# Kernel optimization log

Measured on AMD Instinct MI355X. Metric: run time of the kernel, lower is better.

Reference implementation:

```python
import jax, jax.numpy as jnp
import numpy as np

N = 1048576   # total nodes
E = 8388608   # total edges
IN = 5        # in_channels
H = 32        # hid_channels
G = 16384     # num graphs
C = 10        # num_classes
L = 2         # conv_unit
EPS = 1e-5


def setup_inputs() -> dict:
    key = jax.random.key(0)
    ks = jax.random.split(key, 16)
    x = jax.random.normal(ks[0], (N, IN), dtype=jnp.float32)
    edge_index = jax.random.randint(ks[1], (2, E), 0, N, dtype=jnp.int64)
    edge_attr = jax.random.uniform(ks[2], (E, 1), dtype=jnp.float32)
    batch = jnp.sort(jax.random.randint(ks[3], (N,), 0, G, dtype=jnp.int64))
    s_in = 1.0 / np.sqrt(IN)
    s_h = 1.0 / np.sqrt(H)
    s_2h = 1.0 / np.sqrt(2 * H)
    W_emb = jax.random.normal(ks[4], (H, IN), dtype=jnp.float32) * s_in
    b_emb = jnp.zeros((H,), dtype=jnp.float32)
    W_rel = jax.random.normal(ks[5], (L, H, H), dtype=jnp.float32) * s_h
    b_rel = jnp.zeros((L, H), dtype=jnp.float32)
    W_root = jax.random.normal(ks[6], (L, H, H), dtype=jnp.float32) * s_h
    bn_gamma = jnp.ones((L, H), dtype=jnp.float32)
    bn_beta = jnp.zeros((L, H), dtype=jnp.float32)
    W1 = jax.random.normal(ks[7], (2 * H, H), dtype=jnp.float32) * s_h
    b1 = jnp.zeros((2 * H,), dtype=jnp.float32)
    W2 = jax.random.normal(ks[8], (C, 2 * H), dtype=jnp.float32) * s_2h
    b2 = jnp.zeros((C,), dtype=jnp.float32)
    return {
        "x": x, "edge_index": edge_index, "edge_attr": edge_attr, "batch": batch,
        "W_emb": W_emb, "b_emb": b_emb, "W_rel": W_rel, "b_rel": b_rel,
        "W_root": W_root, "bn_gamma": bn_gamma, "bn_beta": bn_beta,
        "W1": W1, "b1": b1, "W2": W2, "b2": b2,
    }


def _graph_conv(x, src, dst, ew, Wrel, brel, Wroot):
    # PyG GraphConv: lin_rel(scatter_add(ew * x[src] -> dst)) + lin_root(x)
    msg = x[src] * ew[:, None]                              # [E, H]
    agg = jax.ops.segment_sum(msg, dst, num_segments=N)     # [N, H]
    return agg @ Wrel.T + brel + x @ Wroot.T


def _batch_norm(x, gamma, beta):
    mean = jnp.mean(x, axis=0)
    var = jnp.mean(jnp.square(x - mean), axis=0)  # biased, as torch training BN
    return (x - mean) * jax.lax.rsqrt(var + EPS) * gamma + beta


def reference(x, edge_index, edge_attr, batch, W_emb, b_emb, W_rel, b_rel,
              W_root, bn_gamma, bn_beta, W1, b1, W2, b2):
    src, dst = edge_index[0], edge_index[1]
    ew = edge_attr.reshape(-1)
    h = x @ W_emb.T + b_emb                                  # node_emb
    for i in range(L):
        h = _graph_conv(h, src, dst, ew, W_rel[i], b_rel[i], W_root[i])
        h = jax.nn.relu(_batch_norm(h, bn_gamma[i], bn_beta[i]))
    graph_x = jax.ops.segment_max(h, batch, num_segments=G)  # global_max_pool
    hidden = jax.nn.relu(graph_x @ W1.T + b1)
    return hidden @ W2.T + b2                                # [G, C]
```

## Files before the change

kernel.cpp:

```cpp
#include <hip/hip_runtime.h>
#include <hip/hip_fp16.h>

#define NN 1048576
#define NE 8388608
#define NG 16384
#define NBUCK 256
#define BSH 12
#define EPB (NE / 256)

typedef _Float16 half8 __attribute__((ext_vector_type(8)));
typedef float f32x16 __attribute__((ext_vector_type(16)));

__global__ __launch_bounds__(256) void k_embed(const float* __restrict__ x,
    const float* __restrict__ W, const float* __restrict__ b, __half* __restrict__ h) {
  __shared__ float sW[160];
  __shared__ float sb[32];
  int t = threadIdx.x;
  if (t < 160) sW[t] = W[t];
  if (t < 32) sb[t] = b[t];
  __syncthreads();
  int idx = blockIdx.x * 256 + t;
  int c = idx & 31, n = idx >> 5;
  const float* xr = x + n * 5;
  float acc = sb[c];
#pragma unroll
  for (int k = 0; k < 5; ++k) acc = fmaf(xr[k], sW[c * 5 + k], acc);
  h[idx] = __float2half(acc);
}

__global__ __launch_bounds__(256) void k_pcnt(const int* __restrict__ dst, int* __restrict__ hist) {
  __shared__ int lh[NBUCK];
  int t = threadIdx.x;
  lh[t] = 0;
  __syncthreads();
  int base = blockIdx.x * EPB;
  for (int e = base + t; e < base + EPB; e += 256)
    atomicAdd(&lh[dst[e] >> BSH], 1);
  __syncthreads();
  hist[t * 256 + blockIdx.x] = lh[t];
}

__global__ __launch_bounds__(256) void k_scanA(int* __restrict__ hist, int* __restrict__ tot) {
  __shared__ int s2[256];
  int b = blockIdx.x, t = threadIdx.x;
  int v = hist[b * 256 + t];
  s2[t] = v; __syncthreads();
  for (int st = 1; st < 256; st <<= 1) {
    int a = (t >= st) ? s2[t - st] : 0; __syncthreads(); s2[t] += a; __syncthreads();
  }
  hist[b * 256 + t] = s2[t] - v;
  if (t == 255) tot[b] = s2[255];
}

__global__ __launch_bounds__(256) void k_scanB(const int* __restrict__ tot, int* __restrict__ gbase) {
  __shared__ int s2[256];
  int t = threadIdx.x;
  int c = tot[t];
  s2[t] = c; __syncthreads();
  for (int st = 1; st < 256; st <<= 1) {
    int a = (t >= st) ? s2[t - st] : 0; __syncthreads(); s2[t] += a; __syncthreads();
  }
  gbase[t] = s2[t] - c;
  if (t == 255) gbase[256] = s2[255];
}

__global__ __launch_bounds__(256) void k_part(const int* __restrict__ ei, const float* __restrict__ ew,
                                              const int* __restrict__ hist, const int* __restrict__ gbase,
                                              uint2* __restrict__ bsw) {
  __shared__ int cur[NBUCK];
  int t = threadIdx.x, blk = blockIdx.x;
  cur[t] = gbase[t] + hist[t * 256 + blk];
  __syncthreads();
  int base = blk * EPB;
  for (int e = base + t; e < base + EPB; e += 256) {
    int src = ei[e];
    int d   = ei[NE + e];
    unsigned wb = __float_as_uint(ew[e]);
    int b = d >> BSH;
    int pos = atomicAdd(&cur[b], 1);
    bsw[pos] = make_uint2(((unsigned)src << 12) | (unsigned)(d & 4095), wb);
  }
}

__global__ __launch_bounds__(256) void k_fillD(const int* __restrict__ gbase, const uint2* __restrict__ bsw,
                                               int* __restrict__ rowptr, uint2* __restrict__ colw) {
  __shared__ int loc[4096];
  __shared__ int s2[256];
  int t = threadIdx.x, b = blockIdx.x;
  int beg = gbase[b], end = gbase[b + 1], gb = beg;
  int node_base = b << BSH;
#pragma unroll
  for (int j = 0; j < 16; ++j) loc[t * 16 + j] = 0;
  __syncthreads();
  for (int i = beg + t; i < end; i += 256) atomicAdd(&loc[bsw[i].x & 4095], 1);
  __syncthreads();
  int v[16]; int tsum = 0;
#pragma unroll
  for (int j = 0; j < 16; ++j) { v[j] = loc[t * 16 + j]; tsum += v[j]; }
  s2[t] = tsum; __syncthreads();
  for (int st = 1; st < 256; st <<= 1) {
    int a = (t >= st) ? s2[t - st] : 0; __syncthreads(); s2[t] += a; __syncthreads();
  }
  int run = s2[t] - tsum;
#pragma unroll
  for (int j = 0; j < 16; ++j) {
    loc[t * 16 + j] = run;
    rowptr[node_base + t * 16 + j] = gb + run;
    run += v[j];
  }
  if (b == NBUCK - 1 && t == 255) rowptr[NN] = NE;
  __syncthreads();
  for (int i = beg + t; i < end; i += 256) {
    uint2 r = bsw[i];
    int p = atomicAdd(&loc[r.x & 4095], 1);
    colw[gb + p] = make_uint2(r.x >> 12, r.y);
  }
}

__global__ __launch_bounds__(256) void k_gbound(const int* __restrict__ batch, int* __restrict__ gptr) {
  int n = blockIdx.x * 256 + threadIdx.x;
  int b = batch[n];
  int prev = (n == 0) ? -1 : batch[n - 1];
  for (int g = prev + 1; g <= b; ++g) gptr[g] = n;
  if (n == NN - 1) {
    for (int g = b + 1; g <= NG; ++g) gptr[g] = NN;
  }
}

template <int FUSE_BN>
__global__ __launch_bounds__(256) void k_agglin(
    const int* __restrict__ rowptr, const uint2* __restrict__ colw,
    const __half* __restrict__ hIn, const float* __restrict__ bnss,
    const float* __restrict__ Wrel, const float* __restrict__ brel,
    const float* __restrict__ Wroot, __half* __restrict__ hPre,
    double* __restrict__ stats) {
  __shared__ __half sA[4][1024];
  __shared__ uint2 sE[256];
  __shared__ float sBn[64];
  __shared__ double rS[256], rQ[256];
  int t = threadIdx.x;
  int wv = t >> 6, lane = t & 63;
  int c = lane & 31, hi = lane >> 5, grp = t >> 5;
  char* myA = (char*)sA[wv];

  if (FUSE_BN && t < 64) sBn[t] = bnss[t];
  __syncthreads();

  float bs0 = 0.f, bs1 = 0.f;
  if constexpr (FUSE_BN) { bs0 = bnss[c]; bs1 = bnss[32 + c]; }

  half8 bfr[4];
#pragma unroll
  for (int m = 0; m < 4; ++m)
#pragma unroll
    for (int j = 0; j < 8; ++j) {
      int k = 16 * m + hi * 8 + j;
      float w = (k < 32) ? Wrel[c * 32 + k] : Wroot[c * 32 + (k - 32)];
      bfr[m][j] = (_Float16)w;
    }
  float bias = brel[c];
  double aS = 0.0, aQ = 0.0;

  for (int tile = blockIdx.x * 4 + wv; tile < NN / 32; tile += gridDim.x * 4) {
    int nbase = tile * 32;
    for (int r = 0; r < 16; ++r) {
      int node = 2 * r + hi;
      int n = nbase + node;
      int r0 = rowptr[n], r1 = rowptr[n + 1];
      float acc = 0.f;
      for (int j = r0; j < r1; j += 32) {
        int m_ = r1 - j; if (m_ > 32) m_ = 32;
        uint2 cw = make_uint2(0u, 0u);
        if (c < m_) cw = colw[j + c];
        sE[t] = cw;
        int mm = (m_ + 7) & ~7;
        for (int i = 0; i < mm; i += 8) {
          const uint4* eb4 = (const uint4*)&sE[grp * 32 + i];
          uint4 q0 = eb4[0], q1 = eb4[1], q2 = eb4[2], q3 = eb4[3];
          float h0 = __half2float(hIn[(size_t)q0.x * 32 + c]);
          float h1 = __half2float(hIn[(size_t)q0.z * 32 + c]);
          float h2 = __half2float(hIn[(size_t)q1.x * 32 + c]);
          float h3 = __half2float(hIn[(size_t)q1.z * 32 + c]);
          float h4 = __half2float(hIn[(size_t)q2.x * 32 + c]);
          float h5 = __half2float(hIn[(size_t)q2.z * 32 + c]);
          float h6 = __half2float(hIn[(size_t)q3.x * 32 + c]);
          float h7 = __half2float(hIn[(size_t)q3.z * 32 + c]);
          if constexpr (FUSE_BN) {
            h0 = fmaxf(fmaf(h0, bs0, bs1), 0.f);
            h1 = fmaxf(fmaf(h1, bs0, bs1), 0.f);
            h2 = fmaxf(fmaf(h2, bs0, bs1), 0.f);
            h3 = fmaxf(fmaf(h3, bs0, bs1), 0.f);
            h4 = fmaxf(fmaf(h4, bs0, bs1), 0.f);
            h5 = fmaxf(fmaf(h5, bs0, bs1), 0.f);
            h6 = fmaxf(fmaf(h6, bs0, bs1), 0.f);
            h7 = fmaxf(fmaf(h7, bs0, bs1), 0.f);
          }
          acc = fmaf(__uint_as_float(q0.y), h0, acc);
          acc = fmaf(__uint_as_float(q0.w), h1, acc);
          acc = fmaf(__uint_as_float(q1.y), h2, acc);
          acc = fmaf(__uint_as_float(q1.w), h3, acc);
          acc = fmaf(__uint_as_float(q2.y), h4, acc);
          acc = fmaf(__uint_as_float(q2.w), h5, acc);
          acc = fmaf(__uint_as_float(q3.y), h6, acc);
          acc = fmaf(__uint_as_float(q3.w), h7, acc);
        }
      }
      int bw = (node * 64 + c * 2) ^ ((node & 7) << 4);
      *(__half*)(myA + bw) = __float2half(acc);
    }
    f32x16 d;
#pragma unroll
    for (int r = 0; r < 16; ++r) d[r] = bias;
#pragma unroll
    for (int m = 0; m < 4; ++m) {
      half8 a;
      if (m < 2) {
        int node = c;
        int br = (node * 64 + (16 * m + hi * 8) * 2) ^ ((node & 7) << 4);
        a = *(const half8*)(myA + br);
      } else {
        int chb = 16 * (m - 2) + hi * 8;
        a = *(const half8*)(hIn + (size_t)(nbase + c) * 32 + chb);
        if constexpr (FUSE_BN) {
#pragma unroll
          for (int j = 0; j < 8; ++j) {
            float v = (float)a[j];
            v = fmaxf(fmaf(v, sBn[chb + j], sBn[32 + chb + j]), 0.f);
            a[j] = (_Float16)v;
          }
        }
      }
      d = __builtin_amdgcn_mfma_f32_32x32x16_f16(a, bfr[m], d, 0, 0, 0);
    }
#pragma unroll
    for (int r = 0; r < 16; ++r) {
      int node = (r & 3) + 8 * (r >> 2) + 4 * hi;
      float v = d[r];
      hPre[(size_t)(nbase + node) * 32 + c] = __float2half(v);
      aS += v; aQ += (double)v * v;
    }
  }
  rS[t] = aS; rQ[t] = aQ;
  __syncthreads();
  for (int s = 128; s >= 32; s >>= 1) {
    if (t < s) { rS[t] += rS[t + s]; rQ[t] += rQ[t + s]; }
    __syncthreads();
  }
  if (t < 32) {
    atomicAdd(&stats[t], rS[t]);
    atomicAdd(&stats[32 + t], rQ[t]);
  }
}

__global__ void k_bnfin(const double* __restrict__ stats, const float* __restrict__ gamma,
                        const float* __restrict__ beta, float* __restrict__ ss) {
  int c = threadIdx.x;
  double mean = stats[c] * (1.0 / NN);
  double var = stats[32 + c] * (1.0 / NN) - mean * mean;
  float scale = gamma[c] * (float)(1.0 / sqrt(var + 1e-5));
  ss[c] = scale;
  ss[32 + c] = beta[c] - (float)mean * scale;
}

__global__ __launch_bounds__(256) void k_pool(const __half* __restrict__ hB,
    const float* __restrict__ ss, const int* __restrict__ gptr, float* __restrict__ pooled) {
  int t = threadIdx.x;
  int wv = t >> 6, lane = t & 63;
  int p = lane >> 4, cl = lane & 15;
  float s0x = ss[2 * cl], s0y = ss[2 * cl + 1];
  float s1x = ss[32 + 2 * cl], s1y = ss[32 + 2 * cl + 1];
  int g = blockIdx.x * 4 + wv;
  int a = gptr[g], b = gptr[g + 1];
  float mx = 0.f, my = 0.f;
  for (int n = a + p; n < b; n += 4) {
    float2 hv = __half22float2(*(const __half2*)(hB + (size_t)n * 32 + 2 * cl));
    mx = fmaxf(mx, fmaf(hv.x, s0x, s1x));
    my = fmaxf(my, fmaf(hv.y, s0y, s1y));
  }
  mx = fmaxf(mx, __shfl_xor(mx, 16, 64)); my = fmaxf(my, __shfl_xor(my, 16, 64));
  mx = fmaxf(mx, __shfl_xor(mx, 32, 64)); my = fmaxf(my, __shfl_xor(my, 32, 64));
  if (p == 0) *(float2*)&pooled[g * 32 + 2 * cl] = make_float2(mx, my);
}

__global__ __launch_bounds__(256) void k_head(const float* __restrict__ pooled,
    const float* __restrict__ W1, const float* __restrict__ b1,
    const float* __restrict__ W2, const float* __restrict__ b2, float* __restrict__ out) {
  __shared__ float sW1[64 * 33], sW2[10 * 65], sb1[64], sb2[10];
  __shared__ float sHid[4][64];
  int t = threadIdx.x;
  for (int i = t; i < 2048; i += 256) sW1[(i >> 5) * 33 + (i & 31)] = W1[i];
  for (int i = t; i < 640; i += 256) sW2[(i >> 6) * 65 + (i & 63)] = W2[i];
  if (t < 64) sb1[t] = b1[t];
  if (t < 10) sb2[t] = b2[t];
  __syncthreads();
  int w = t >> 6, lane = t & 63;
  for (int g = blockIdx.x * 4 + w; g < NG; g += gridDim.x * 4) {
    float pv = (lane < 32) ? pooled[g * 32 + lane] : 0.f;
    float acc = sb1[lane];
#pragma unroll
    for (int k = 0; k < 32; ++k)
      acc = fmaf(__shfl(pv, k, 64), sW1[lane * 33 + k], acc);
    acc = fmaxf(acc, 0.f);
    sHid[w][lane] = acc;
    __syncthreads();
    if (lane < 10) {
      float o = sb2[lane];
#pragma unroll
      for (int j = 0; j < 64; ++j) o = fmaf(sHid[w][j], sW2[lane * 65 + j], o);
      out[g * 10 + lane] = o;
    }
    __syncthreads();
  }
}

extern "C" void kernel_launch(void* const* d_in, const int* in_sizes, int n_in,
                              void* d_out, int out_size, void* d_ws, size_t ws_size,
                              hipStream_t stream) {
  const float* x      = (const float*)d_in[0];
  const int*   ei     = (const int*)d_in[1];
  const float* ea     = (const float*)d_in[2];
  const int*   batch  = (const int*)d_in[3];
  const float* W_emb  = (const float*)d_in[4];
  const float* b_emb  = (const float*)d_in[5];
  const float* W_rel  = (const float*)d_in[6];
  const float* b_rel  = (const float*)d_in[7];
  const float* W_root = (const float*)d_in[8];
  const float* gamma  = (const float*)d_in[9];
  const float* beta   = (const float*)d_in[10];
  const float* W1     = (const float*)d_in[11];
  const float* b1     = (const float*)d_in[12];
  const float* W2     = (const float*)d_in[13];
  const float* b2     = (const float*)d_in[14];
  float* out = (float*)d_out;

  char* ws = (char*)d_ws;
  size_t off = 0;
  __half* hA    = (__half*)(ws + off); off += (size_t)NN * 32 * 2;
  uint2*  colw  = (uint2*)(ws + off);  off += (size_t)NE * 8;
  uint2*  bsw   = (uint2*)(ws + off);
  __half* hB    = (__half*)(ws + off);
  off += (size_t)NE * 8;
  int*    rowptr= (int*)(ws + off);    off += ((size_t)NN + 64) * 4;
  int*    hist  = (int*)(ws + off);    off += (size_t)NBUCK * 256 * 4;
  int*    tot   = (int*)(ws + off);    off += 1024;
  int*    gbase = (int*)(ws + off);    off += 2048;
  int*    gptr  = (int*)(ws + off);    off += ((size_t)NG + 64) * 4;
  float*  pooled= (float*)(ws + off);
  double* stats = (double*)d_out;
  float*  ss0   = (float*)((char*)d_out + 512);
  float*  ss1   = (float*)((char*)d_out + 768);

  k_embed<<<NN * 32 / 256, 256, 0, stream>>>(x, W_emb, b_emb, hA);

  k_pcnt <<<256, 256, 0, stream>>>(ei + NE, hist);
  k_scanA<<<NBUCK, 256, 0, stream>>>(hist, tot);
  k_scanB<<<1, 256, 0, stream>>>(tot, gbase);
  k_part <<<256, 256, 0, stream>>>(ei, ea, hist, gbase, bsw);
  k_fillD<<<NBUCK, 256, 0, stream>>>(gbase, bsw, rowptr, colw);
  k_gbound<<<NN / 256, 256, 0, stream>>>(batch, gptr);

  (void)hipMemsetAsync(stats, 0, 64 * 8, stream);
  k_agglin<0><<<2048, 256, 0, stream>>>(rowptr, colw, hA, nullptr,
                                        W_rel, b_rel, W_root, hB, stats);
  k_bnfin<<<1, 32, 0, stream>>>(stats, gamma, beta, ss0);

  (void)hipMemsetAsync(stats, 0, 64 * 8, stream);
  k_agglin<1><<<2048, 256, 0, stream>>>(rowptr, colw, hB, ss0,
                                        W_rel + 1024, b_rel + 32, W_root + 1024, hA, stats);
  k_bnfin<<<1, 32, 0, stream>>>(stats, gamma + 32, beta + 32, ss1);

  k_pool<<<NG / 4, 256, 0, stream>>>(hA, ss1, gptr, pooled);
  k_head<<<1024, 256, 0, stream>>>(pooled, W1, b1, W2, b2, out);
}
```

Before: 1.007 ms.

## Prefetch rowptr and next node's edge chunk; use float per-thread BN stats

```diff
diff --git a/kernel.cpp b/kernel.cpp
--- a/kernel.cpp
+++ b/kernel.cpp
@@ -128,7 +128,7 @@
 }
 
 template <int FUSE_BN>
-__global__ __launch_bounds__(256) void k_agglin(
+__global__ __launch_bounds__(256, 8) void k_agglin(
     const int* __restrict__ rowptr, const uint2* __restrict__ colw,
     const __half* __restrict__ hIn, const float* __restrict__ bnss,
     const float* __restrict__ Wrel, const float* __restrict__ brel,
@@ -159,20 +159,30 @@
       bfr[m][j] = (_Float16)w;
     }
   float bias = brel[c];
-  double aS = 0.0, aQ = 0.0;
+  float aS = 0.f, aQ = 0.f;
 
   for (int tile = blockIdx.x * 4 + wv; tile < NN / 32; tile += gridDim.x * 4) {
     int nbase = tile * 32;
+    int rp = 0;
+    if (lane < 33) rp = rowptr[nbase + lane];
+    int r0 = __shfl(rp, hi, 64);
+    int r1 = __shfl(rp, hi + 1, 64);
+    uint2 cw = make_uint2(0u, 0u);
+    { int m_ = r1 - r0; if (m_ > 32) m_ = 32; if (c < m_) cw = colw[r0 + c]; }
+
     for (int r = 0; r < 16; ++r) {
-      int node = 2 * r + hi;
-      int n = nbase + node;
-      int r0 = rowptr[n], r1 = rowptr[n + 1];
+      sE[t] = cw;
+      int sr0 = r0, sr1 = r1;
+      if (r < 15) {
+        r0 = __shfl(rp, 2 * (r + 1) + hi, 64);
+        r1 = __shfl(rp, 2 * (r + 1) + hi + 1, 64);
+        cw = make_uint2(0u, 0u);
+        int m_ = r1 - r0; if (m_ > 32) m_ = 32;
+        if (c < m_) cw = colw[r0 + c];
+      }
       float acc = 0.f;
-      for (int j = r0; j < r1; j += 32) {
-        int m_ = r1 - j; if (m_ > 32) m_ = 32;
-        uint2 cw = make_uint2(0u, 0u);
-        if (c < m_) cw = colw[j + c];
-        sE[t] = cw;
+      {
+        int m_ = sr1 - sr0; if (m_ > 32) m_ = 32;
         int mm = (m_ + 7) & ~7;
         for (int i = 0; i < mm; i += 8) {
           const uint4* eb4 = (const uint4*)&sE[grp * 32 + i];
@@ -186,14 +196,10 @@
           float h6 = __half2float(hIn[(size_t)q3.x * 32 + c]);
           float h7 = __half2float(hIn[(size_t)q3.z * 32 + c]);
           if constexpr (FUSE_BN) {
-            h0 = fmaxf(fmaf(h0, bs0, bs1), 0.f);
-            h1 = fmaxf(fmaf(h1, bs0, bs1), 0.f);
-            h2 = fmaxf(fmaf(h2, bs0, bs1), 0.f);
-            h3 = fmaxf(fmaf(h3, bs0, bs1), 0.f);
-            h4 = fmaxf(fmaf(h4, bs0, bs1), 0.f);
-            h5 = fmaxf(fmaf(h5, bs0, bs1), 0.f);
-            h6 = fmaxf(fmaf(h6, bs0, bs1), 0.f);
-            h7 = fmaxf(fmaf(h7, bs0, bs1), 0.f);
+            h0 = fmaxf(fmaf(h0, bs0, bs1), 0.f); h1 = fmaxf(fmaf(h1, bs0, bs1), 0.f);
+            h2 = fmaxf(fmaf(h2, bs0, bs1), 0.f); h3 = fmaxf(fmaf(h3, bs0, bs1), 0.f);
+            h4 = fmaxf(fmaf(h4, bs0, bs1), 0.f); h5 = fmaxf(fmaf(h5, bs0, bs1), 0.f);
+            h6 = fmaxf(fmaf(h6, bs0, bs1), 0.f); h7 = fmaxf(fmaf(h7, bs0, bs1), 0.f);
           }
           acc = fmaf(__uint_as_float(q0.y), h0, acc);
           acc = fmaf(__uint_as_float(q0.w), h1, acc);
@@ -205,6 +211,40 @@
           acc = fmaf(__uint_as_float(q3.w), h7, acc);
         }
       }
+      for (int j = sr0 + 32; j < sr1; j += 32) {
+        int m_ = sr1 - j; if (m_ > 32) m_ = 32;
+        uint2 cw2 = make_uint2(0u, 0u);
+        if (c < m_) cw2 = colw[j + c];
+        sE[t] = cw2;
+        int mm = (m_ + 7) & ~7;
+        for (int i = 0; i < mm; i += 8) {
+          const uint4* eb4 = (const uint4*)&sE[grp * 32 + i];
+          uint4 q0 = eb4[0], q1 = eb4[1], q2 = eb4[2], q3 = eb4[3];
+          float h0 = __half2float(hIn[(size_t)q0.x * 32 + c]);
+          float h1 = __half2float(hIn[(size_t)q0.z * 32 + c]);
+          float h2 = __half2float(hIn[(size_t)q1.x * 32 + c]);
+          float h3 = __half2float(hIn[(size_t)q1.z * 32 + c]);
+          float h4 = __half2float(hIn[(size_t)q2.x * 32 + c]);
+          float h5 = __half2float(hIn[(size_t)q2.z * 32 + c]);
+          float h6 = __half2float(hIn[(size_t)q3.x * 32 + c]);
+          float h7 = __half2float(hIn[(size_t)q3.z * 32 + c]);
+          if constexpr (FUSE_BN) {
+            h0 = fmaxf(fmaf(h0, bs0, bs1), 0.f); h1 = fmaxf(fmaf(h1, bs0, bs1), 0.f);
+            h2 = fmaxf(fmaf(h2, bs0, bs1), 0.f); h3 = fmaxf(fmaf(h3, bs0, bs1), 0.f);
+            h4 = fmaxf(fmaf(h4, bs0, bs1), 0.f); h5 = fmaxf(fmaf(h5, bs0, bs1), 0.f);
+            h6 = fmaxf(fmaf(h6, bs0, bs1), 0.f); h7 = fmaxf(fmaf(h7, bs0, bs1), 0.f);
+          }
+          acc = fmaf(__uint_as_float(q0.y), h0, acc);
+          acc = fmaf(__uint_as_float(q0.w), h1, acc);
+          acc = fmaf(__uint_as_float(q1.y), h2, acc);
+          acc = fmaf(__uint_as_float(q1.w), h3, acc);
+          acc = fmaf(__uint_as_float(q2.y), h4, acc);
+          acc = fmaf(__uint_as_float(q2.w), h5, acc);
+          acc = fmaf(__uint_as_float(q3.y), h6, acc);
+          acc = fmaf(__uint_as_float(q3.w), h7, acc);
+        }
+      }
+      int node = 2 * r + hi;
       int bw = (node * 64 + c * 2) ^ ((node & 7) << 4);
       *(__half*)(myA + bw) = __float2half(acc);
     }
@@ -237,10 +277,10 @@
       int node = (r & 3) + 8 * (r >> 2) + 4 * hi;
       float v = d[r];
       hPre[(size_t)(nbase + node) * 32 + c] = __float2half(v);
-      aS += v; aQ += (double)v * v;
+      aS += v; aQ += v * v;
     }
   }
-  rS[t] = aS; rQ[t] = aQ;
+  rS[t] = (double)aS; rQ[t] = (double)aQ;
   __syncthreads();
   for (int s = 128; s >= 32; s >>= 1) {
     if (t < s) { rS[t] += rS[t + s]; rQ[t] += rQ[t + s]; }
```

After: 1.028 ms. 2.1% more time.
